# Kernel tuning notes

Measured on AMD Instinct MI355X. Metric: run time of the kernel, lower is better.

The kernel has to match this reference:

```python
import jax, jax.numpy as jnp
import numpy as np

B, F, D = 4096, 39, 16
L0, L1 = 128, 128
H1 = L0 // 2  # split_half: half the maps feed the next layer


def setup_inputs() -> dict:
    key = jax.random.key(0)
    k0, k1, k2, k3, k4 = jax.random.split(key, 5)
    x = jax.random.normal(k0, (B, F, D), dtype=jnp.float32)
    # Conv1D(size, 1, channels_first) == matmul over channel dim: W [out, in]
    W0 = jax.random.normal(k1, (L0, F * F), dtype=jnp.float32) * 0.02
    b0 = jnp.zeros((L0,), dtype=jnp.float32)
    W1 = jax.random.normal(k2, (L1, H1 * F), dtype=jnp.float32) * 0.02
    b1 = jnp.zeros((L1,), dtype=jnp.float32)
    return {"x": x, "W0": W0, "b0": b0, "W1": W1, "b1": b1}


def _cin_layer(h, h0, W, b):
    # h: [B, H, D], h0: [B, F, D] -> outer product [B, H*F, D], then 1x1 conv
    z = jnp.einsum('bhd,bmd->bhmd', h, h0)
    z = z.reshape(z.shape[0], -1, z.shape[-1])          # [B, H*F, D]
    y = jnp.einsum('oc,bcd->bod', W, z) + b[None, :, None]
    return jax.nn.relu(y)


def reference(x, W0, b0, W1, b1):
    h0 = x
    # layer 0 (split_half, not last): split into next_hidden / direct_connect
    y0 = _cin_layer(h0, h0, W0, b0)                     # [B, L0, D]
    next_hidden, direct0 = y0[:, :H1, :], y0[:, H1:, :]
    # layer 1 (last): all maps are direct connect
    direct1 = _cin_layer(next_hidden, h0, W1, b1)       # [B, L1, D]
    result = jnp.sum(jnp.concatenate([direct0, direct1], axis=1), axis=-1)
    return result  # [B, L0//2 + L1]
```

## Files before the change

kernel.cpp:

```cpp
#include <hip/hip_runtime.h>
#include <hip/hip_fp16.h>
#include <stdint.h>

#define B_     4096
#define F_     39
#define KKPAD  133
#define WPANEL ((size_t)KKPAD * 1024)

typedef _Float16 f16x8  __attribute__((ext_vector_type(8)));
typedef float    f32x4  __attribute__((ext_vector_type(4)));
typedef float    f32x16 __attribute__((ext_vector_type(16)));

union FragAB { f16x8 h8; __half2 h2[4]; f32x4 f4; unsigned u[4]; __half h[8]; };

__device__ __forceinline__ void gload_lds16(const void* g, void* l) {
    __builtin_amdgcn_global_load_lds(
        (const __attribute__((address_space(1))) void*)g,
        (__attribute__((address_space(3))) void*)l, 16, 0, 0);
}

__global__ __launch_bounds__(256) void prep_w(
    const float* __restrict__ W0, const float* __restrict__ W1,
    __half* __restrict__ Wp)
{
    int idx = blockIdx.x * 256 + threadIdx.x;
    if (idx >= 4 * 130 * 1024) return;
    int j    = idx & 7;
    int lane = (idx >> 3) & 63;
    int ks   = (idx >> 9) & 1;
    int rest = idx >> 10;
    int kk   = rest % 130, Mt = rest / 130;
    int o    = Mt * 32 + (lane & 31);
    int sub  = lane >> 5;
    float v = 0.f;
    if (kk < 50) {
        int seg = kk / 10, kkin = kk - seg * 10;
        int h = 4 * kkin + 2 * ks + sub;
        int m = seg * 8 + j;
        if (h < 39 && m < 39) v = W0[o * 1521 + h * 39 + m];
    } else {
        int l = kk - 50;
        int seg = l / 10, kkin = l - seg * 10;
        int m = 4 * kkin + 2 * ks + sub;
        int h = seg * 8 + j;
        if (m < 39) v = W1[o * 2496 + h * 39 + m];
    }
    Wp[(size_t)Mt * WPANEL + ((size_t)kk * 2 + ks) * 512 + lane * 8 + j] = __float2half(v);
}

__device__ __forceinline__ void inner10(
    const __half* gpf, __half* As, int lane,
    const FragAB (&xmc)[4][5], const FragAB (&xcur)[4],
    f32x16 (&acc)[4], unsigned psel)
{
#pragma unroll
    for (int kkin = 0; kkin < 10; ++kkin) {
        const int slot = kkin % 5;

        asm volatile("s_waitcnt vmcnt(4)" ::: "memory");

        FragAB A0, A1;
        A0.f4 = *(const f32x4*)(As + slot * 1024 + lane * 8);
        A1.f4 = *(const f32x4*)(As + slot * 1024 + 512 + lane * 8);

#pragma unroll
        for (int ks = 0; ks < 2; ++ks) {
            const int ee = 2 * kkin + ks;
#pragma unroll
            for (int p = 0; p < 4; ++p) {
                unsigned bc = __builtin_amdgcn_perm(0u, xmc[p][ee >> 2].u[ee & 3], psel);
                __half2 xh2 = *(__half2*)&bc;
                FragAB bfr;
#pragma unroll
                for (int q = 0; q < 4; ++q)
                    bfr.h2[q] = __hmul2(xcur[p].h2[q], xh2);
                acc[p] = __builtin_amdgcn_mfma_f32_32x32x16_f16(
                    (ks ? A1 : A0).h8, bfr.h8, acc[p], 0, 0, 0);
            }
        }

        {
            const __half* g = gpf + kkin * 1024 + lane * 8;
            const int ws = ((kkin + 3) % 5) * 1024;
            gload_lds16(g,       As + ws);
            gload_lds16(g + 512, As + ws + 512);
        }
    }
}

__global__ __launch_bounds__(256, 2) void cin_main(
    const float* __restrict__ x, const float* __restrict__ b0,
    const float* __restrict__ b1, const __half* __restrict__ Wp,
    float* __restrict__ out)
{
    __shared__ __align__(16) __half Asl[4][5][1024];
    __shared__ __align__(16) __half xT[8][16][40];
    __shared__ __align__(16) __half nhT[8][16][72];
    __shared__ float bs0[128], bs1[128];

    const int t    = threadIdx.x;
    const int w    = t >> 6, lane = t & 63;
    const int sub  = lane >> 5, bp = (lane >> 4) & 1, d = lane & 15;
    const int gb   = blockIdx.x * 8;

    __half* As = &Asl[w][0][0];
    const __half* gp = Wp + (size_t)w * WPANEL;

#pragma unroll
    for (int k0 = 0; k0 < 3; ++k0) {
        const __half* g = gp + (size_t)k0 * 1024 + lane * 8;
        gload_lds16(g,       As + k0 * 1024);
        gload_lds16(g + 512, As + k0 * 1024 + 512);
    }

    if (t < 128) { bs0[t] = b0[t]; bs1[t] = b1[t]; }

    for (int i = t; i < 1248; i += 256) {
        int bt = i / 156, r2 = i - bt * 156;
        int f = r2 >> 2, dq = r2 & 3;
        float4 v = *(const float4*)&x[((size_t)(gb + bt) * F_ + f) * 16 + dq * 4];
        xT[bt][dq * 4 + 0][f] = __float2half(v.x);
        xT[bt][dq * 4 + 1][f] = __float2half(v.y);
        xT[bt][dq * 4 + 2][f] = __float2half(v.z);
        xT[bt][dq * 4 + 3][f] = __float2half(v.w);
    }
    if (t < 128) xT[t >> 4][t & 15][39] = __float2half(0.f);
    __syncthreads();

    FragAB xmc[4][5];
#pragma unroll
    for (int p = 0; p < 4; ++p)
#pragma unroll
        for (int a = 0; a < 5; ++a)
            xmc[p][a].f4 = *(const f32x4*)&xT[2 * p + bp][d][a * 8];

    const unsigned psel = sub ? 0x03020302u : 0x01000100u;

    f32x16 acc[4];
#pragma unroll
    for (int r = 0; r < 16; ++r) {
        float bv = bs0[w * 32 + (r & 3) + 8 * (r >> 2) + 4 * sub];
#pragma unroll
        for (int p = 0; p < 4; ++p) acc[p][r] = bv;
    }

    const __half* gpf = gp + (size_t)3 * 1024;
#pragma unroll 1
    for (int s = 0; s < 5; ++s) {
        FragAB xcur[4];
#pragma unroll
        for (int p = 0; p < 4; ++p)
            xcur[p].f4 = *(const f32x4*)(&xT[2 * p + bp][d][0] + s * 8);
        inner10(gpf, As, lane, xmc, xcur, acc, psel);
        gpf += 10 * 1024;
    }

    if (w < 2) {
#pragma unroll
        for (int p = 0; p < 4; ++p) {
            __half* nr = &nhT[2 * p + bp][d][0];
#pragma unroll
            for (int rq = 0; rq < 4; ++rq) {
                union { __half h[4]; float2 f2; } pk;
#pragma unroll
                for (int q = 0; q < 4; ++q)
                    pk.h[q] = __float2half(fmaxf(acc[p][rq * 4 + q], 0.f));
                *(float2*)(nr + w * 32 + 8 * rq + 4 * sub) = pk.f2;
            }
        }
    } else {
#pragma unroll
        for (int p = 0; p < 4; ++p) {
#pragma unroll
            for (int rq = 0; rq < 4; ++rq) {
                float4 s4; float* sv = (float*)&s4;
#pragma unroll
                for (int q = 0; q < 4; ++q) {
                    float v = fmaxf(acc[p][rq * 4 + q], 0.f);
                    v += __shfl_xor(v, 1); v += __shfl_xor(v, 2);
                    v += __shfl_xor(v, 4); v += __shfl_xor(v, 8);
                    sv[q] = v;
                }
                if (d == 0) {
                    int row = w * 32 + 8 * rq + 4 * sub;
                    *(float4*)&out[(size_t)(gb + 2 * p + bp) * 192 + (row - 64)] = s4;
                }
            }
        }
    }
#pragma unroll
    for (int r = 0; r < 16; ++r) {
        float bv = bs1[w * 32 + (r & 3) + 8 * (r >> 2) + 4 * sub];
#pragma unroll
        for (int p = 0; p < 4; ++p) acc[p][r] = bv;
    }
    __syncthreads();

#pragma unroll 1
    for (int s = 0; s < 8; ++s) {
        FragAB xcur[4];
#pragma unroll
        for (int p = 0; p < 4; ++p)
            xcur[p].f4 = *(const f32x4*)(&nhT[2 * p + bp][d][0] + s * 8);
        inner10(gpf, As, lane, xmc, xcur, acc, psel);
        gpf += 10 * 1024;
    }

#pragma unroll
    for (int p = 0; p < 4; ++p) {
#pragma unroll
        for (int rq = 0; rq < 4; ++rq) {
            float4 s4; float* sv = (float*)&s4;
#pragma unroll
            for (int q = 0; q < 4; ++q) {
                float v = fmaxf(acc[p][rq * 4 + q], 0.f);
                v += __shfl_xor(v, 1); v += __shfl_xor(v, 2);
                v += __shfl_xor(v, 4); v += __shfl_xor(v, 8);
                sv[q] = v;
            }
            if (d == 0) {
                int row = w * 32 + 8 * rq + 4 * sub;
                *(float4*)&out[(size_t)(gb + 2 * p + bp) * 192 + 64 + row] = s4;
            }
        }
    }
}

extern "C" void kernel_launch(void* const* d_in, const int* in_sizes, int n_in,
                              void* d_out, int out_size, void* d_ws, size_t ws_size,
                              hipStream_t stream) {
    const float* x  = (const float*)d_in[0];
    const float* W0 = (const float*)d_in[1];
    const float* b0 = (const float*)d_in[2];
    const float* W1 = (const float*)d_in[3];
    const float* b1 = (const float*)d_in[4];
    float* out = (float*)d_out;
    __half* Wp = (__half*)d_ws;

    prep_w<<<(4 * 130 * 1024 + 255) / 256, 256, 0, stream>>>(W0, W1, Wp);
    cin_main<<<B_ / 8, 256, 0, stream>>>(x, b0, b1, Wp, out);
}
```

Measured before the change: 75.20 us.

## Retile warps to 2x2 M-by-batch blocks and load weights directly to registers

Each warp now computes two 32-row output tiles across two batch pairs instead of one tile across four pairs. Each B fragment (the x-scaled product) is reused across two MFMAs, which halves the hmul2 work per MFMA. Weight fragments come straight from global memory into a double-buffered register pipeline, replacing the LDS ring filled by global_load_lds. The broadcast x scalars are precomputed once into registers rather than permuted inside the loop. Each weight panel is now read by two warps per block, so global/L2 traffic for weights roughly doubles, and the global loads are less deeply prefetched.

```diff
diff --git a/kernel.cpp b/kernel.cpp
--- a/kernel.cpp
+++ b/kernel.cpp
@@ -12,12 +12,6 @@
 typedef float    f32x16 __attribute__((ext_vector_type(16)));
 
 union FragAB { f16x8 h8; __half2 h2[4]; f32x4 f4; unsigned u[4]; __half h[8]; };
-
-__device__ __forceinline__ void gload_lds16(const void* g, void* l) {
-    __builtin_amdgcn_global_load_lds(
-        (const __attribute__((address_space(1))) void*)g,
-        (__attribute__((address_space(3))) void*)l, 16, 0, 0);
-}
 
 __global__ __launch_bounds__(256) void prep_w(
     const float* __restrict__ W0, const float* __restrict__ W1,
@@ -48,43 +42,40 @@
     Wp[(size_t)Mt * WPANEL + ((size_t)kk * 2 + ks) * 512 + lane * 8 + j] = __float2half(v);
 }
 
-__device__ __forceinline__ void inner10(
-    const __half* gpf, __half* As, int lane,
-    const FragAB (&xmc)[4][5], const FragAB (&xcur)[4],
-    f32x16 (&acc)[4], unsigned psel)
+__device__ __forceinline__ void seg10(
+    const __half* pA, const __half* pB,
+    FragAB (&An)[2][2][2],
+    const __half2 (&xsc)[2][20],
+    const FragAB (&xcur)[2],
+    f32x16 (&acc)[2][2])
 {
 #pragma unroll
     for (int kkin = 0; kkin < 10; ++kkin) {
-        const int slot = kkin % 5;
-
-        asm volatile("s_waitcnt vmcnt(4)" ::: "memory");
-
-        FragAB A0, A1;
-        A0.f4 = *(const f32x4*)(As + slot * 1024 + lane * 8);
-        A1.f4 = *(const f32x4*)(As + slot * 1024 + 512 + lane * 8);
+        const int s = kkin & 1;
 
 #pragma unroll
         for (int ks = 0; ks < 2; ++ks) {
             const int ee = 2 * kkin + ks;
-#pragma unroll
-            for (int p = 0; p < 4; ++p) {
-                unsigned bc = __builtin_amdgcn_perm(0u, xmc[p][ee >> 2].u[ee & 3], psel);
-                __half2 xh2 = *(__half2*)&bc;
-                FragAB bfr;
+            FragAB bfr[2];
+#pragma unroll
+            for (int p = 0; p < 2; ++p) {
+                const __half2 xs = xsc[p][ee];
 #pragma unroll
                 for (int q = 0; q < 4; ++q)
-                    bfr.h2[q] = __hmul2(xcur[p].h2[q], xh2);
-                acc[p] = __builtin_amdgcn_mfma_f32_32x32x16_f16(
-                    (ks ? A1 : A0).h8, bfr.h8, acc[p], 0, 0, 0);
+                    bfr[p].h2[q] = __hmul2(xcur[p].h2[q], xs);
             }
-        }
-
-        {
-            const __half* g = gpf + kkin * 1024 + lane * 8;
-            const int ws = ((kkin + 3) % 5) * 1024;
-            gload_lds16(g,       As + ws);
-            gload_lds16(g + 512, As + ws + 512);
-        }
+#pragma unroll
+            for (int mt = 0; mt < 2; ++mt)
+#pragma unroll
+                for (int p = 0; p < 2; ++p)
+                    acc[mt][p] = __builtin_amdgcn_mfma_f32_32x32x16_f16(
+                        An[s][mt][ks].h8, bfr[p].h8, acc[mt][p], 0, 0, 0);
+        }
+
+        An[s][0][0].f4 = *(const f32x4*)(pA + (kkin + 2) * 1024);
+        An[s][0][1].f4 = *(const f32x4*)(pA + (kkin + 2) * 1024 + 512);
+        An[s][1][0].f4 = *(const f32x4*)(pB + (kkin + 2) * 1024);
+        An[s][1][1].f4 = *(const f32x4*)(pB + (kkin + 2) * 1024 + 512);
     }
 }
 
@@ -93,24 +84,26 @@
     const float* __restrict__ b1, const __half* __restrict__ Wp,
     float* __restrict__ out)
 {
-    __shared__ __align__(16) __half Asl[4][5][1024];
     __shared__ __align__(16) __half xT[8][16][40];
     __shared__ __align__(16) __half nhT[8][16][72];
     __shared__ float bs0[128], bs1[128];
 
     const int t    = threadIdx.x;
     const int w    = t >> 6, lane = t & 63;
+    const int mp   = w & 1, g = w >> 1;
     const int sub  = lane >> 5, bp = (lane >> 4) & 1, d = lane & 15;
     const int gb   = blockIdx.x * 8;
 
-    __half* As = &Asl[w][0][0];
-    const __half* gp = Wp + (size_t)w * WPANEL;
-
-#pragma unroll
-    for (int k0 = 0; k0 < 3; ++k0) {
-        const __half* g = gp + (size_t)k0 * 1024 + lane * 8;
-        gload_lds16(g,       As + k0 * 1024);
-        gload_lds16(g + 512, As + k0 * 1024 + 512);
+    const __half* gA = Wp + (size_t)(2 * mp) * WPANEL + lane * 8;
+    const __half* gB = gA + WPANEL;
+
+    FragAB An[2][2][2];
+#pragma unroll
+    for (int k0 = 0; k0 < 2; ++k0) {
+        An[k0][0][0].f4 = *(const f32x4*)(gA + (size_t)k0 * 1024);
+        An[k0][0][1].f4 = *(const f32x4*)(gA + (size_t)k0 * 1024 + 512);
+        An[k0][1][0].f4 = *(const f32x4*)(gB + (size_t)k0 * 1024);
+        An[k0][1][1].f4 = *(const f32x4*)(gB + (size_t)k0 * 1024 + 512);
     }
 
     if (t < 128) { bs0[t] = b0[t]; bs1[t] = b1[t]; }
@@ -127,103 +120,120 @@
     if (t < 128) xT[t >> 4][t & 15][39] = __float2half(0.f);
     __syncthreads();
 
-    FragAB xmc[4][5];
-#pragma unroll
-    for (int p = 0; p < 4; ++p)
-#pragma unroll
-        for (int a = 0; a < 5; ++a)
-            xmc[p][a].f4 = *(const f32x4*)&xT[2 * p + bp][d][a * 8];
-
+    const __half* xrow0 = &xT[4 * g + bp][d][0];
+    const __half* xrow1 = &xT[4 * g + 2 + bp][d][0];
     const unsigned psel = sub ? 0x03020302u : 0x01000100u;
 
-    f32x16 acc[4];
-#pragma unroll
-    for (int r = 0; r < 16; ++r) {
-        float bv = bs0[w * 32 + (r & 3) + 8 * (r >> 2) + 4 * sub];
-#pragma unroll
-        for (int p = 0; p < 4; ++p) acc[p][r] = bv;
-    }
-
-    const __half* gpf = gp + (size_t)3 * 1024;
+    __half2 xsc[2][20];
+#pragma unroll
+    for (int a = 0; a < 5; ++a) {
+        FragAB t0, t1;
+        t0.f4 = *(const f32x4*)(xrow0 + a * 8);
+        t1.f4 = *(const f32x4*)(xrow1 + a * 8);
+#pragma unroll
+        for (int b = 0; b < 4; ++b) {
+            unsigned c0 = __builtin_amdgcn_perm(0u, t0.u[b], psel);
+            unsigned c1 = __builtin_amdgcn_perm(0u, t1.u[b], psel);
+            xsc[0][4 * a + b] = *(__half2*)&c0;
+            xsc[1][4 * a + b] = *(__half2*)&c1;
+        }
+    }
+
+    f32x16 acc[2][2];
+#pragma unroll
+    for (int mt = 0; mt < 2; ++mt)
+#pragma unroll
+        for (int r = 0; r < 16; ++r) {
+            float bv = bs0[(2 * mp + mt) * 32 + (r & 3) + 8 * (r >> 2) + 4 * sub];
+            acc[mt][0][r] = bv; acc[mt][1][r] = bv;
+        }
+
+    FragAB xcur[2];
+
 #pragma unroll 1
     for (int s = 0; s < 5; ++s) {
-        FragAB xcur[4];
-#pragma unroll
-        for (int p = 0; p < 4; ++p)
-            xcur[p].f4 = *(const f32x4*)(&xT[2 * p + bp][d][0] + s * 8);
-        inner10(gpf, As, lane, xmc, xcur, acc, psel);
-        gpf += 10 * 1024;
-    }
-
-    if (w < 2) {
-#pragma unroll
-        for (int p = 0; p < 4; ++p) {
-            __half* nr = &nhT[2 * p + bp][d][0];
-#pragma unroll
-            for (int rq = 0; rq < 4; ++rq) {
-                union { __half h[4]; float2 f2; } pk;
-#pragma unroll
-                for (int q = 0; q < 4; ++q)
-                    pk.h[q] = __float2half(fmaxf(acc[p][rq * 4 + q], 0.f));
-                *(float2*)(nr + w * 32 + 8 * rq + 4 * sub) = pk.f2;
+        xcur[0].f4 = *(const f32x4*)(xrow0 + s * 8);
+        xcur[1].f4 = *(const f32x4*)(xrow1 + s * 8);
+        seg10(gA + (size_t)s * 10240, gB + (size_t)s * 10240, An, xsc, xcur, acc);
+    }
+
+    if (mp == 0) {
+#pragma unroll
+        for (int mt = 0; mt < 2; ++mt)
+#pragma unroll
+            for (int p = 0; p < 2; ++p) {
+                __half* nr = &nhT[4 * g + 2 * p + bp][d][0];
+#pragma unroll
+                for (int rq = 0; rq < 4; ++rq) {
+                    union { __half h[4]; float2 f2; } pk;
+#pragma unroll
+                    for (int q = 0; q < 4; ++q)
+                        pk.h[q] = __float2half(fmaxf(acc[mt][p][rq * 4 + q], 0.f));
+                    *(float2*)(nr + mt * 32 + 8 * rq + 4 * sub) = pk.f2;
+                }
             }
-        }
     } else {
 #pragma unroll
-        for (int p = 0; p < 4; ++p) {
+        for (int mt = 0; mt < 2; ++mt)
+#pragma unroll
+            for (int p = 0; p < 2; ++p)
+#pragma unroll
+                for (int rq = 0; rq < 4; ++rq) {
+                    float4 s4; float* sv = (float*)&s4;
+#pragma unroll
+                    for (int q = 0; q < 4; ++q) {
+                        float v = fmaxf(acc[mt][p][rq * 4 + q], 0.f);
+                        v += __shfl_xor(v, 1); v += __shfl_xor(v, 2);
+                        v += __shfl_xor(v, 4); v += __shfl_xor(v, 8);
+                        sv[q] = v;
+                    }
+                    if (d == 0) {
+                        int row = (2 + mt) * 32 + 8 * rq + 4 * sub;
+                        int b   = gb + 4 * g + 2 * p + bp;
+                        *(float4*)&out[(size_t)b * 192 + (row - 64)] = s4;
+                    }
+                }
+    }
+#pragma unroll
+    for (int mt = 0; mt < 2; ++mt)
+#pragma unroll
+        for (int r = 0; r < 16; ++r) {
+            float bv = bs1[(2 * mp + mt) * 32 + (r & 3) + 8 * (r >> 2) + 4 * sub];
+            acc[mt][0][r] = bv; acc[mt][1][r] = bv;
+        }
+    __syncthreads();
+
+    const __half* nrow0 = &nhT[4 * g + bp][d][0];
+    const __half* nrow1 = &nhT[4 * g + 2 + bp][d][0];
+    const __half* gA1 = gA + (size_t)50 * 1024;
+    const __half* gB1 = gB + (size_t)50 * 1024;
+#pragma unroll 1
+    for (int s = 0; s < 8; ++s) {
+        xcur[0].f4 = *(const f32x4*)(nrow0 + s * 8);
+        xcur[1].f4 = *(const f32x4*)(nrow1 + s * 8);
+        seg10(gA1 + (size_t)s * 10240, gB1 + (size_t)s * 10240, An, xsc, xcur, acc);
+    }
+
+#pragma unroll
+    for (int mt = 0; mt < 2; ++mt)
+#pragma unroll
+        for (int p = 0; p < 2; ++p)
 #pragma unroll
             for (int rq = 0; rq < 4; ++rq) {
                 float4 s4; float* sv = (float*)&s4;
 #pragma unroll
                 for (int q = 0; q < 4; ++q) {
-                    float v = fmaxf(acc[p][rq * 4 + q], 0.f);
+                    float v = fmaxf(acc[mt][p][rq * 4 + q], 0.f);
                     v += __shfl_xor(v, 1); v += __shfl_xor(v, 2);
                     v += __shfl_xor(v, 4); v += __shfl_xor(v, 8);
                     sv[q] = v;
                 }
                 if (d == 0) {
-                    int row = w * 32 + 8 * rq + 4 * sub;
-                    *(float4*)&out[(size_t)(gb + 2 * p + bp) * 192 + (row - 64)] = s4;
+                    int row = (2 * mp + mt) * 32 + 8 * rq + 4 * sub;
+                    int b   = gb + 4 * g + 2 * p + bp;
+                    *(float4*)&out[(size_t)b * 192 + 64 + row] = s4;
                 }
             }
-        }
-    }
-#pragma unroll
-    for (int r = 0; r < 16; ++r) {
-        float bv = bs1[w * 32 + (r & 3) + 8 * (r >> 2) + 4 * sub];
-#pragma unroll
-        for (int p = 0; p < 4; ++p) acc[p][r] = bv;
-    }
-    __syncthreads();
-
-#pragma unroll 1
-    for (int s = 0; s < 8; ++s) {
-        FragAB xcur[4];
-#pragma unroll
-        for (int p = 0; p < 4; ++p)
-            xcur[p].f4 = *(const f32x4*)(&nhT[2 * p + bp][d][0] + s * 8);
-        inner10(gpf, As, lane, xmc, xcur, acc, psel);
-        gpf += 10 * 1024;
-    }
-
-#pragma unroll
-    for (int p = 0; p < 4; ++p) {
-#pragma unroll
-        for (int rq = 0; rq < 4; ++rq) {
-            float4 s4; float* sv = (float*)&s4;
-#pragma unroll
-            for (int q = 0; q < 4; ++q) {
-                float v = fmaxf(acc[p][rq * 4 + q], 0.f);
-                v += __shfl_xor(v, 1); v += __shfl_xor(v, 2);
-                v += __shfl_xor(v, 4); v += __shfl_xor(v, 8);
-                sv[q] = v;
-            }
-            if (d == 0) {
-                int row = w * 32 + 8 * rq + 4 * sub;
-                *(float4*)&out[(size_t)(gb + 2 * p + bp) * 192 + 64 + row] = s4;
-            }
-        }
-    }
 }
 
 extern "C" void kernel_launch(void* const* d_in, const int* in_sizes, int n_in,
```

Result: slower. 89.79 us (+19.4%).
